# Kernel optimization log

Hardware: AMD Instinct MI355X
Metric: run time of the kernel (lower is better)

Reference implementation:

```python
import jax, jax.numpy as jnp
import numpy as np

COMPLEXES = 2048
RESX = 16
RESY = 16
RATE = 16
FEAT = 64


def setup_inputs() -> dict:
    key = jax.random.key(0)
    k1, k2, k3 = jax.random.split(key, 3)
    P = RATE * RATE  # samples per complex
    map_ = jax.random.normal(k1, (COMPLEXES, RESY, RESX, FEAT), dtype=jnp.float32)
    u = jax.random.uniform(k2, (COMPLEXES, P), dtype=jnp.float32)
    v = jax.random.uniform(k3, (COMPLEXES, P), dtype=jnp.float32)
    return {"map": map_, "u": u, "v": v}


def reference(map, u, v):
    # map: [complexes, resy, resx, feat]; u, v: [complexes, P] in [0,1]
    C, H, W, F = map.shape
    x = u * (W - 1)
    y = v * (H - 1)
    x0 = jnp.clip(jnp.floor(x).astype(jnp.int32), 0, W - 2)
    y0 = jnp.clip(jnp.floor(y).astype(jnp.int32), 0, H - 2)
    fx = (x - x0.astype(x.dtype))[..., None]  # [C, P, 1]
    fy = (y - y0.astype(y.dtype))[..., None]
    cidx = jnp.arange(C)[:, None]  # [C, 1] broadcast over samples
    g00 = map[cidx, y0, x0]          # [C, P, F]
    g01 = map[cidx, y0, x0 + 1]
    g10 = map[cidx, y0 + 1, x0]
    g11 = map[cidx, y0 + 1, x0 + 1]
    top = g00 * (1.0 - fx) + g01 * fx
    bot = g10 * (1.0 - fx) + g11 * fx
    return top * (1.0 - fy) + bot * fy  # [C, P, F]
```

## Files before the change

kernel.cpp:

```cpp
#include <hip/hip_runtime.h>

constexpr int C_ = 2048;
constexpr int H_ = 16;
constexpr int W_ = 16;
constexpr int F_ = 64;
constexpr int P_ = 256;
constexpr int MAP4 = H_ * W_ * F_ / 4;

__global__ __launch_bounds__(256) void ngf_fetch_kernel(
    const float* __restrict__ map_,
    const float* __restrict__ u_,
    const float* __restrict__ v_,
    float* __restrict__ out_) {
  __shared__ float4 smap[MAP4];
  __shared__ float s_fx[P_];
  __shared__ float s_fy[P_];
  __shared__ int   s_ix[P_];

  const int c = blockIdx.x;
  const int tid = threadIdx.x;

  const float4* gmap = (const float4*)(map_ + (size_t)c * (H_ * W_ * F_));
#pragma unroll
  for (int i = 0; i < MAP4 / 256; ++i) {
    smap[i * 256 + tid] = gmap[i * 256 + tid];
  }

  {
    const float x = u_[(size_t)c * P_ + tid] * (float)(W_ - 1);
    const float y = v_[(size_t)c * P_ + tid] * (float)(H_ - 1);
    int x0 = (int)floorf(x);
    int y0 = (int)floorf(y);
    x0 = x0 < 0 ? 0 : (x0 > W_ - 2 ? W_ - 2 : x0);
    y0 = y0 < 0 ? 0 : (y0 > H_ - 2 ? H_ - 2 : y0);
    s_fx[tid] = x - (float)x0;
    s_fy[tid] = y - (float)y0;
    s_ix[tid] = (y0 * W_ + x0) * (F_ / 4);
  }
  __syncthreads();

  float4* gout = (float4*)(out_ + (size_t)c * (P_ * F_));
  const int f = tid & 15;
  const int sbase = tid >> 4;

#pragma unroll
  for (int it = 0; it < 16; ++it) {
    const int s = it * 16 + sbase;
    const float fx = s_fx[s];
    const float fy = s_fy[s];
    const int ix = s_ix[s] + f;

    const float4 g00 = smap[ix];
    const float4 g01 = smap[ix + (F_ / 4)];
    const float4 g10 = smap[ix + W_ * (F_ / 4)];
    const float4 g11 = smap[ix + (W_ + 1) * (F_ / 4)];

    const float wx1 = fx, wx0 = 1.0f - fx;
    const float wy1 = fy, wy0 = 1.0f - fy;

    float4 r;
    r.x = (g00.x * wx0 + g01.x * wx1) * wy0 + (g10.x * wx0 + g11.x * wx1) * wy1;
    r.y = (g00.y * wx0 + g01.y * wx1) * wy0 + (g10.y * wx0 + g11.y * wx1) * wy1;
    r.z = (g00.z * wx0 + g01.z * wx1) * wy0 + (g10.z * wx0 + g11.z * wx1) * wy1;
    r.w = (g00.w * wx0 + g01.w * wx1) * wy0 + (g10.w * wx0 + g11.w * wx1) * wy1;

    gout[s * (F_ / 4) + f] = r;
  }
}

extern "C" void kernel_launch(void* const* d_in, const int* in_sizes, int n_in,
                              void* d_out, int out_size, void* d_ws, size_t ws_size,
                              hipStream_t stream) {
  const float* map_ = (const float*)d_in[0];
  const float* u_   = (const float*)d_in[1];
  const float* v_   = (const float*)d_in[2];
  float* out_ = (float*)d_out;

  ngf_fetch_kernel<<<C_, 256, 0, stream>>>(map_, u_, v_, out_);
}
```

Baseline: 239.2 us.

## Gather bilinear taps directly from global memory instead of staging map in LDS

Removes the per-block copy of the whole 64KB feature map into shared memory and instead reads the four corner taps directly from global memory, relying on L1/L2 caching. Precomputes the four bilinear weights per sample as a float4 in shared memory, so the inner loop does four FMAs per channel. This shrinks LDS use from about 67KB to about 5KB, which should raise occupancy, at the risk of redundant global/L2 traffic on repeated tap reads.

```diff
diff --git a/kernel.cpp b/kernel.cpp
--- a/kernel.cpp
+++ b/kernel.cpp
@@ -5,26 +5,17 @@
 constexpr int W_ = 16;
 constexpr int F_ = 64;
 constexpr int P_ = 256;
-constexpr int MAP4 = H_ * W_ * F_ / 4;
 
 __global__ __launch_bounds__(256) void ngf_fetch_kernel(
     const float* __restrict__ map_,
     const float* __restrict__ u_,
     const float* __restrict__ v_,
     float* __restrict__ out_) {
-  __shared__ float4 smap[MAP4];
-  __shared__ float s_fx[P_];
-  __shared__ float s_fy[P_];
-  __shared__ int   s_ix[P_];
+  __shared__ float4 s_w[P_];
+  __shared__ int    s_ix[P_];
 
   const int c = blockIdx.x;
   const int tid = threadIdx.x;
-
-  const float4* gmap = (const float4*)(map_ + (size_t)c * (H_ * W_ * F_));
-#pragma unroll
-  for (int i = 0; i < MAP4 / 256; ++i) {
-    smap[i * 256 + tid] = gmap[i * 256 + tid];
-  }
 
   {
     const float x = u_[(size_t)c * P_ + tid] * (float)(W_ - 1);
@@ -33,36 +24,37 @@
     int y0 = (int)floorf(y);
     x0 = x0 < 0 ? 0 : (x0 > W_ - 2 ? W_ - 2 : x0);
     y0 = y0 < 0 ? 0 : (y0 > H_ - 2 ? H_ - 2 : y0);
-    s_fx[tid] = x - (float)x0;
-    s_fy[tid] = y - (float)y0;
+    const float fx = x - (float)x0;
+    const float fy = y - (float)y0;
+    const float wx0 = 1.0f - fx;
+    const float wy0 = 1.0f - fy;
+    s_w[tid] = make_float4(wx0 * wy0, fx * wy0, wx0 * fy, fx * fy);
     s_ix[tid] = (y0 * W_ + x0) * (F_ / 4);
   }
   __syncthreads();
 
-  float4* gout = (float4*)(out_ + (size_t)c * (P_ * F_));
+  const float4* __restrict__ gmap =
+      (const float4*)(map_ + (size_t)c * (H_ * W_ * F_));
+  float4* __restrict__ gout = (float4*)(out_ + (size_t)c * (P_ * F_));
   const int f = tid & 15;
   const int sbase = tid >> 4;
 
 #pragma unroll
   for (int it = 0; it < 16; ++it) {
     const int s = it * 16 + sbase;
-    const float fx = s_fx[s];
-    const float fy = s_fy[s];
+    const float4 w = s_w[s];
     const int ix = s_ix[s] + f;
 
-    const float4 g00 = smap[ix];
-    const float4 g01 = smap[ix + (F_ / 4)];
-    const float4 g10 = smap[ix + W_ * (F_ / 4)];
-    const float4 g11 = smap[ix + (W_ + 1) * (F_ / 4)];
-
-    const float wx1 = fx, wx0 = 1.0f - fx;
-    const float wy1 = fy, wy0 = 1.0f - fy;
+    const float4 g00 = gmap[ix];
+    const float4 g01 = gmap[ix + (F_ / 4)];
+    const float4 g10 = gmap[ix + W_ * (F_ / 4)];
+    const float4 g11 = gmap[ix + (W_ + 1) * (F_ / 4)];
 
     float4 r;
-    r.x = (g00.x * wx0 + g01.x * wx1) * wy0 + (g10.x * wx0 + g11.x * wx1) * wy1;
-    r.y = (g00.y * wx0 + g01.y * wx1) * wy0 + (g10.y * wx0 + g11.y * wx1) * wy1;
-    r.z = (g00.z * wx0 + g01.z * wx1) * wy0 + (g10.z * wx0 + g11.z * wx1) * wy1;
-    r.w = (g00.w * wx0 + g01.w * wx1) * wy0 + (g10.w * wx0 + g11.w * wx1) * wy1;
+    r.x = g00.x * w.x + g01.x * w.y + g10.x * w.z + g11.x * w.w;
+    r.y = g00.y * w.x + g01.y * w.y + g10.y * w.z + g11.y * w.w;
+    r.z = g00.z * w.x + g01.z * w.y + g10.z * w.z + g11.z * w.w;
+    r.w = g00.w * w.x + g01.w * w.y + g10.w * w.z + g11.w * w.w;
 
     gout[s * (F_ / 4) + f] = r;
   }
```

Result: slower. 260.0 us (+8.7%).
